# Kernel tuning notes

Hardware: AMD Instinct MI355X
Metric: run time of the kernel (lower is better)

## Reference

```python
import jax, jax.numpy as jnp
import numpy as np

IN_FEATURES = 1024
OUT_FEATURES = 64
DEGREE = 3
NUM_KNOTS = 10
BATCH = 8192
K0 = NUM_KNOTS + DEGREE  # number of basis columns / control points per edge


def b_spline_basis(x, knots, degree):
    """Vectorized Cox-de Boor recursion.
    x: (..., ) values in [0,1]; knots: (K0+1,).
    Returns (..., K0) basis; last `degree` columns are zero-padded (matches
    control_points width of num_knots+degree as in the original module).
    """
    t = knots
    n0 = t.shape[0] - 1  # = K0 degree-0 intervals
    xe = x[..., None]
    basis = ((xe >= t[:-1]) & (xe < t[1:])).astype(x.dtype)  # (..., K0)
    for p in range(1, degree + 1):
        ti = t[: n0 - p]
        tip = t[p:n0]
        ti1 = t[1 : n0 - p + 1]
        tip1 = t[p + 1 : n0 + 1]
        d1 = jnp.where(tip - ti > 0, tip - ti, jnp.ones_like(ti))
        d2 = jnp.where(tip1 - ti1 > 0, tip1 - ti1, jnp.ones_like(ti1))
        left = jnp.where(tip - ti > 0, (xe - ti) / d1, 0.0) * basis[..., : n0 - p]
        right = jnp.where(tip1 - ti1 > 0, (tip1 - xe) / d2, 0.0) * basis[..., 1 : n0 - p + 1]
        new = left + right
        pad = jnp.zeros(x.shape + (p,), x.dtype)
        basis = jnp.concatenate([new, pad], axis=-1)
    return basis


def setup_inputs() -> dict:
    key = jax.random.key(0)
    k1, k2 = jax.random.split(key)
    x = jax.random.uniform(k1, (BATCH, IN_FEATURES), dtype=jnp.float32)
    knots = jnp.linspace(0.0, 1.0, NUM_KNOTS + DEGREE + 1, dtype=jnp.float32)
    control_points = jax.random.normal(k2, (OUT_FEATURES, IN_FEATURES, K0), dtype=jnp.float32)
    return {"x": x, "knots": knots, "control_points": control_points}


def reference(x, knots, control_points):
    # basis: (B, in, K0) computed once per input feature (original recomputes
    # it out_features times inside a double loop -- same math, fused here).
    basis = b_spline_basis(x, knots, DEGREE)
    # outputs[b, o] = sum_j sum_k basis[b, j, k] * control_points[o, j, k]
    return jnp.einsum("bjk,ojk->bo", basis, control_points)
```

## Files before the change

### kernel.cpp

```cpp
#include <hip/hip_runtime.h>
#include <hip/hip_bf16.h>
#include <stdint.h>

#define IN_F   1024
#define OUT_F  64
#define BATCH  8192
#define BM     256
#define NTHR   512
#define JSPLIT 32
#define JPB    (IN_F / JSPLIT)
#define JC     4
#define NCH    (JPB / JC)
#define BT_B   (JC * 2048)
#define TBL_B  (14 * 32 * 48)
#define XSTG_B (BM * JPB * 4)
#define LDS_T  (TBL_B + XSTG_B + 2 * BT_B)
#define OUTSZ  (BATCH * OUT_F)

typedef __attribute__((ext_vector_type(8)))  short short8;
typedef __attribute__((ext_vector_type(16))) float f32x16;

__device__ __forceinline__ void gll16(const void* g, void* l) {
    __builtin_amdgcn_global_load_lds(
        (const __attribute__((address_space(1))) uint32_t*)g,
        (__attribute__((address_space(3))) uint32_t*)l,
        16, 0, 0);
}

__global__ void kan_prep(const float* __restrict__ cp, __hip_bfloat16* __restrict__ bt) {
    int j = blockIdx.x * 4 + (threadIdx.x >> 6);
    int o = threadIdx.x & 63;
    const float* src = cp + ((size_t)o * IN_F + j) * 13;
    float v[16];
#pragma unroll
    for (int k = 0; k < 10; ++k) v[k] = src[k];
#pragma unroll
    for (int k = 10; k < 16; ++k) v[k] = 0.0f;
    __hip_bfloat16* dst = bt + (size_t)j * 1024;
#pragma unroll
    for (int kh = 0; kh < 2; ++kh)
#pragma unroll
        for (int e = 0; e < 8; ++e)
            dst[kh * 512 + o * 8 + e] = __float2bfloat16(v[kh * 8 + e]);
}

template<bool PART>
__launch_bounds__(NTHR, 4)
__global__ void kan_main(const float* __restrict__ x,
                         const __hip_bfloat16* __restrict__ bt,
                         void* __restrict__ outp) {
    __shared__ __attribute__((aligned(16))) char lds[LDS_T];

    const int tid   = threadIdx.x;
    const int w     = tid >> 6;
    const int lane  = tid & 63;
    const int l31   = lane & 31;
    const int khalf = lane >> 5;

    const int r0 = blockIdx.x * BM;
    const int j0 = blockIdx.y * JPB;

    const char* btg = (const char*)bt + (size_t)j0 * 2048 + (size_t)tid * 16;
    const char* xlg = (const char*)x + ((size_t)(r0 + lane) * IN_F + j0) * 4;
    const int   wofs = w << 10;

#pragma unroll
    for (int i = 0; i < 4; ++i)
        gll16(xlg + (size_t)(i * 64) * 4096 + w * 16,
              lds + TBL_B + (w << 12) + (i << 10));

#define STAGE_BT(ch, bi) \
    gll16(btg + (size_t)(ch) * BT_B, lds + TBL_B + XSTG_B + (bi) * BT_B + wofs)

    STAGE_BT(0, 0);
    STAGE_BT(1, 1);

    for (int e = tid; e < 14 * 32; e += NTHR) {
        const int m = e >> 5, u5 = e & 31;
        const float uu = (u5 + 0.5f) * (1.0f / 32.0f);
        const float u2 = uu * uu;
        const float omu = 1.0f - uu;
        const float o2 = omu * omu;
        const float B3 = u2 * (uu * (1.0f / 6.0f));
        const float B0 = o2 * (omu * (1.0f / 6.0f));
        const float B1 = __builtin_fmaf(u2, __builtin_fmaf(uu, 0.5f, -1.0f), 2.0f / 3.0f);
        const float B2 = 1.0f - B0 - B1 - B3;
        uint32_t P01, P23;
        asm("v_cvt_pk_bf16_f32 %0, %1, %2" : "=v"(P01) : "v"(B0), "v"(B1));
        asm("v_cvt_pk_bf16_f32 %0, %1, %2" : "=v"(P23) : "v"(B2), "v"(B3));
        const uint64_t V = ((uint64_t)P23 << 32) | (uint64_t)P01;
#pragma unroll
        for (int h = 0; h < 2; ++h) {
            const int c0 = 48 + (h << 7);
            const int p = (m << 4) - c0;
            const uint64_t sl = V << ((uint32_t)p & 63);
            const uint64_t sr = V >> ((uint32_t)(-p) & 63);
            const uint64_t t0 = (p < 0) ? sr : sl;
            const uint64_t q0 = ((uint32_t)(p + 63) < 127u) ? t0 : 0ull;
            const uint64_t t1 = (p < 64) ? sr : sl;
            const uint64_t q1 = ((uint32_t)(p - 16) < 112u) ? t1 : 0ull;
            uint64_t* d = (uint64_t*)(lds + e * 48 + h * 16);
            d[0] = q0; d[1] = q1;
        }
    }

#define AFRAG(xv) ({                                              \
        const float t416_ = (xv) * 416.0f;           \
        const int i_ = (int)t416_;                 \
        const int s_ = ((i_ << 1) + i_) << 4;         \
        *(const short8*)(lds + s_ + (khalf << 4)); })

#define COMPUTE(ch, bi) do {                                                  \
        const char* base = lds + TBL_B + XSTG_B + (bi) * BT_B;                \
        float xa[4];                                                          \
        const char* xr = lds + TBL_B + (ch) * 4096 + (((w << 5) + l31) << 4); \
        *(float4*)xa = *(const float4*)(xr);    \
        const char* bbb = base + (khalf << 10) + l31 * 16;                    \
        _Pragma("unroll")                                                     \
        for (int jl = 0; jl < JC; ++jl) {                                     \
            const short8 b0 = *(const short8*)(bbb + jl * 2048);              \
            const short8 b1 = *(const short8*)(bbb + jl * 2048 + 512);        \
            const short8 a  = AFRAG(xa[jl]);                                  \
            acc0 = __builtin_amdgcn_mfma_f32_32x32x16_bf16(a, b0, acc0, 0, 0, 0); \
            acc1 = __builtin_amdgcn_mfma_f32_32x32x16_bf16(a, b1, acc1, 0, 0, 0); \
        }                                                                     \
    } while (0)

    f32x16 acc0, acc1;
#pragma unroll
    for (int i = 0; i < 16; ++i) { acc0[i] = 0.0f; acc1[i] = 0.0f; }

    __syncthreads();

    int cur = 0;
#pragma unroll 1
    for (int ch = 0; ch < NCH; ++ch) {
        if (ch >= 2) {
            if (ch == NCH - 1) asm volatile("s_waitcnt vmcnt(0)" ::: "memory");
            else               asm volatile("s_waitcnt vmcnt(1)" ::: "memory");
            __builtin_amdgcn_s_barrier();
            __builtin_amdgcn_sched_barrier(0);
        }
        COMPUTE(ch, cur);
        if (ch + 2 < NCH) {
            __builtin_amdgcn_s_barrier();
            __builtin_amdgcn_sched_barrier(0);
            STAGE_BT(ch + 2, cur);
        }
        cur ^= 1;
    }
#undef STAGE_BT
#undef AFRAG
#undef COMPUTE

    if (PART) {
        __hip_bfloat16* op = (__hip_bfloat16*)outp + (size_t)blockIdx.y * OUTSZ;
#pragma unroll
        for (int r = 0; r < 16; ++r) {
            const int crow = (r & 3) + 8 * (r >> 2) + 4 * khalf;
            __hip_bfloat16* p0 = op + (size_t)(r0 + (w << 5) + crow) * OUT_F;
            p0[l31]      = __float2bfloat16(acc0[r]);
            p0[l31 + 32] = __float2bfloat16(acc1[r]);
        }
    } else {
        float* op = (float*)outp;
#pragma unroll
        for (int r = 0; r < 16; ++r) {
            const int crow = (r & 3) + 8 * (r >> 2) + 4 * khalf;
            float* p0 = op + (size_t)(r0 + (w << 5) + crow) * OUT_F;
            atomicAdd(p0 + l31,      acc0[r]);
            atomicAdd(p0 + l31 + 32, acc1[r]);
        }
    }
}

__global__ void kan_reduce(const __hip_bfloat16* __restrict__ part,
                           float* __restrict__ out) {
    const int i = (blockIdx.x * 256 + threadIdx.x) * 4;
    float s0 = 0.0f, s1 = 0.0f, s2 = 0.0f, s3 = 0.0f;
#pragma unroll
    for (int b = 0; b < JSPLIT; ++b) {
        const uint2 v = *(const uint2*)(part + (size_t)b * OUTSZ + i);
        union { uint32_t u; float f; } c0, c1, c2, c3;
        c0.u = v.x << 16;
        c1.u = v.x & 0xffff0000u;
        c2.u = v.y << 16;
        c3.u = v.y & 0xffff0000u;
        s0 += c0.f; s1 += c1.f; s2 += c2.f; s3 += c3.f;
    }
    float4 r = {s0, s1, s2, s3};
    *(float4*)(out + i) = r;
}

extern "C" void kernel_launch(void* const* d_in, const int* in_sizes, int n_in,
                              void* d_out, int out_size, void* d_ws, size_t ws_size,
                              hipStream_t stream) {
    const float* x  = (const float*)d_in[0];
    const float* cp = (const float*)d_in[2];
    float* out = (float*)d_out;
    __hip_bfloat16* bt   = (__hip_bfloat16*)d_ws;
    __hip_bfloat16* part = (__hip_bfloat16*)((char*)d_ws + 2u * 1024u * 1024u);

    const size_t need = 2u * 1024u * 1024u + (size_t)JSPLIT * OUTSZ * 2u;
    const bool use_part = ws_size >= need;

    kan_prep<<<dim3(IN_F / 4), dim3(256), 0, stream>>>(cp, bt);
    if (use_part) {
        kan_main<true><<<dim3(BATCH / BM, JSPLIT), dim3(NTHR), 0, stream>>>(x, bt, (void*)part);
        kan_reduce<<<dim3(OUTSZ / 1024), dim3(256), 0, stream>>>(part, out);
    } else {
        hipMemsetAsync(d_out, 0, (size_t)out_size * sizeof(float), stream);
        kan_main<false><<<dim3(BATCH / BM, JSPLIT), dim3(NTHR), 0, stream>>>(x, bt, (void*)d_out);
    }
}
```

Baseline: 41.08 us.

## Load B fragments directly from global instead of double-buffered LDS staging

Removes the LDS double-buffer for the prepared bf16 control-point tiles and the per-chunk barriers and waitcnts. Each lane now reads its B fragments straight from global memory (L1/L2-resident, 16 KB per block) inside the MFMA loop. This cuts LDS footprint and synchronization, which may allow more occupancy, at the cost of global-load latency sitting directly in the MFMA dependency chain with no explicit prefetch.

```diff
diff --git a/kernel.cpp b/kernel.cpp
--- a/kernel.cpp
+++ b/kernel.cpp
@@ -9,12 +9,9 @@
 #define NTHR   512
 #define JSPLIT 32
 #define JPB    (IN_F / JSPLIT)
-#define JC     4
-#define NCH    (JPB / JC)
-#define BT_B   (JC * 2048)
 #define TBL_B  (14 * 32 * 48)
 #define XSTG_B (BM * JPB * 4)
-#define LDS_T  (TBL_B + XSTG_B + 2 * BT_B)
+#define LDS_T  (TBL_B + XSTG_B)
 #define OUTSZ  (BATCH * OUT_F)
 
 typedef __attribute__((ext_vector_type(8)))  short short8;
@@ -60,20 +57,13 @@
     const int r0 = blockIdx.x * BM;
     const int j0 = blockIdx.y * JPB;
 
-    const char* btg = (const char*)bt + (size_t)j0 * 2048 + (size_t)tid * 16;
     const char* xlg = (const char*)x + ((size_t)(r0 + lane) * IN_F + j0) * 4;
-    const int   wofs = w << 10;
+    const char* btf = (const char*)bt + (size_t)j0 * 2048 + (khalf << 10) + l31 * 16;
 
 #pragma unroll
     for (int i = 0; i < 4; ++i)
         gll16(xlg + (size_t)(i * 64) * 4096 + w * 16,
               lds + TBL_B + (w << 12) + (i << 10));
-
-#define STAGE_BT(ch, bi) \
-    gll16(btg + (size_t)(ch) * BT_B, lds + TBL_B + XSTG_B + (bi) * BT_B + wofs)
-
-    STAGE_BT(0, 0);
-    STAGE_BT(1, 1);
 
     for (int e = tid; e < 14 * 32; e += NTHR) {
         const int m = e >> 5, u5 = e & 31;
@@ -110,48 +100,28 @@
         const int s_ = ((i_ << 1) + i_) << 4;         \
         *(const short8*)(lds + s_ + (khalf << 4)); })
 
-#define COMPUTE(ch, bi) do {                                                  \
-        const char* base = lds + TBL_B + XSTG_B + (bi) * BT_B;                \
-        float xa[4];                                                          \
-        const char* xr = lds + TBL_B + (ch) * 4096 + (((w << 5) + l31) << 4); \
-        *(float4*)xa = *(const float4*)(xr);    \
-        const char* bbb = base + (khalf << 10) + l31 * 16;                    \
-        _Pragma("unroll")                                                     \
-        for (int jl = 0; jl < JC; ++jl) {                                     \
-            const short8 b0 = *(const short8*)(bbb + jl * 2048);              \
-            const short8 b1 = *(const short8*)(bbb + jl * 2048 + 512);        \
-            const short8 a  = AFRAG(xa[jl]);                                  \
-            acc0 = __builtin_amdgcn_mfma_f32_32x32x16_bf16(a, b0, acc0, 0, 0, 0); \
-            acc1 = __builtin_amdgcn_mfma_f32_32x32x16_bf16(a, b1, acc1, 0, 0, 0); \
-        }                                                                     \
-    } while (0)
-
     f32x16 acc0, acc1;
 #pragma unroll
     for (int i = 0; i < 16; ++i) { acc0[i] = 0.0f; acc1[i] = 0.0f; }
 
     __syncthreads();
 
-    int cur = 0;
 #pragma unroll 1
-    for (int ch = 0; ch < NCH; ++ch) {
-        if (ch >= 2) {
-            if (ch == NCH - 1) asm volatile("s_waitcnt vmcnt(0)" ::: "memory");
-            else               asm volatile("s_waitcnt vmcnt(1)" ::: "memory");
-            __builtin_amdgcn_s_barrier();
-            __builtin_amdgcn_sched_barrier(0);
+    for (int ch = 0; ch < JPB / 4; ++ch) {
+        float xa[4];
+        const char* xr = lds + TBL_B + (ch << 12) + (((w << 5) + l31) << 4);
+        *(float4*)xa = *(const float4*)(xr);
+        const char* bj = btf + (size_t)(ch << 2) * 2048;
+#pragma unroll
+        for (int jl = 0; jl < 4; ++jl) {
+            const short8 b0 = *(const short8*)(bj + jl * 2048);
+            const short8 b1 = *(const short8*)(bj + jl * 2048 + 512);
+            const short8 a  = AFRAG(xa[jl]);
+            acc0 = __builtin_amdgcn_mfma_f32_32x32x16_bf16(a, b0, acc0, 0, 0, 0);
+            acc1 = __builtin_amdgcn_mfma_f32_32x32x16_bf16(a, b1, acc1, 0, 0, 0);
         }
-        COMPUTE(ch, cur);
-        if (ch + 2 < NCH) {
-            __builtin_amdgcn_s_barrier();
-            __builtin_amdgcn_sched_barrier(0);
-            STAGE_BT(ch + 2, cur);
-        }
-        cur ^= 1;
     }
-#undef STAGE_BT
 #undef AFRAG
-#undef COMPUTE
 
     if (PART) {
         __hip_bfloat16* op = (__hip_bfloat16*)outp + (size_t)blockIdx.y * OUTSZ;
```

New measurement: 45.11 us. 9.8% more time.
